# Optimization experiments

Measured on AMD Instinct MI355X. Metric: run time of the kernel, lower is better.

Reference implementation:

```python
import jax, jax.numpy as jnp
import numpy as np

LR = 0.1  # inner-loop learning rate from `param - 0.1 * grad`

D = 4096          # memory width d; key/val are (1, d) per docstring
CTX = 512         # loss_context_size: number of keys per update step


def setup_inputs() -> dict:
    key = jax.random.key(0)
    k1, k2, k3 = jax.random.split(key, 3)
    W = jax.random.normal(k1, (D, D), dtype=jnp.float32) / np.sqrt(D)
    keys = jax.random.normal(k2, (CTX, D), dtype=jnp.float32)
    vals = jax.random.normal(k3, (CTX, D), dtype=jnp.float32)
    return {"W": W, "keys": keys, "vals": vals}


def reference(W, keys, vals):
    # OneStep.forward: preds_i = functional_forward(key_i, (W,)) = key_i @ W,
    # loss = MSE(preds, vals); new_W = W - 0.1 * dloss/dW.
    # The per-key loop is batched into a single (CTX, D) x (D, D) matmul.
    def loss_fn(Wp):
        preds = keys @ Wp  # (CTX, D)
        return jnp.mean((preds - vals) ** 2)

    g = jax.grad(loss_fn)(W)
    return W - LR * g
```

## Files before the change

kernel.cpp:

```cpp
#include <hip/hip_runtime.h>
#include <hip/hip_bf16.h>


typedef __bf16 bf16_t;
typedef __bf16 bf16x8 __attribute__((ext_vector_type(8)));
typedef float f32x4 __attribute__((ext_vector_type(4)));

#define D_DIM 4096
#define CTX_N 512
#define UPD_SCALE 9.5367431640625e-8f

__device__ __forceinline__ void gld16(const bf16_t* g, bf16_t* l) {
    __builtin_amdgcn_global_load_lds(
        (const __attribute__((address_space(1))) void*)g,
        (__attribute__((address_space(3))) void*)l, 16, 0, 0);
}

__device__ __forceinline__ void t_body2(
    float* tile, const float* __restrict__ src, bf16_t* __restrict__ dstT,
    bf16_t* __restrict__ dstN, int M, int N, int bx, int by)
{
    const int tid = threadIdx.x;
    const int C0 = bx * 64, R0 = by * 64;
    const int r  = tid >> 2, cs = (tid & 3) * 16;

    const float* s = src + (size_t)(R0 + r) * N + C0 + cs;
    float f[16];
#pragma unroll
    for (int u = 0; u < 4; ++u) {
        const float4 v = ((const float4*)s)[u];
        f[4 * u + 0] = v.x; f[4 * u + 1] = v.y; f[4 * u + 2] = v.z; f[4 * u + 3] = v.w;
    }
#pragma unroll
    for (int u = 0; u < 16; ++u) tile[r * 65 + cs + u] = f[u];

    if (dstN) {
        bf16x8 v0, v1;
#pragma unroll
        for (int u = 0; u < 8; ++u) { v0[u] = (bf16_t)f[u]; v1[u] = (bf16_t)f[8 + u]; }
        bf16_t* d = dstN + (size_t)(R0 + r) * N + C0 + cs;
        *(bf16x8*)d = v0; *(bf16x8*)(d + 8) = v1;
    }
    __syncthreads();

    bf16x8 o0, o1;
#pragma unroll
    for (int u = 0; u < 8; ++u) {
        o0[u] = (bf16_t)tile[(cs + u) * 65 + r];
        o1[u] = (bf16_t)tile[(cs + 8 + u) * 65 + r];
    }
    bf16_t* d = dstT + (size_t)(C0 + r) * M + R0 + cs;
    *(bf16x8*)d = o0; *(bf16x8*)(d + 8) = o1;
}

__global__ __launch_bounds__(256) void t_all(
    const float* __restrict__ W, const float* __restrict__ K,
    const float* __restrict__ V, bf16_t* __restrict__ Wt,
    bf16_t* __restrict__ Kt, bf16_t* __restrict__ Kb, bf16_t* __restrict__ Vt)
{
    __shared__ float tile[64 * 65];
    const int y = blockIdx.y;
    if (y < 64)      t_body2(tile, W, Wt, nullptr, D_DIM, D_DIM, blockIdx.x, y);
    else if (y < 72) t_body2(tile, K, Kt, Kb,      CTX_N, D_DIM, blockIdx.x, y - 64);
    else             t_body2(tile, V, Vt, nullptr, CTX_N, D_DIM, blockIdx.x, y - 72);
}



__global__ __launch_bounds__(256, 2) void k1_residual(
    const bf16_t* __restrict__ Wt, const bf16_t* __restrict__ Kb,
    const bf16_t* __restrict__ Vt, bf16_t* __restrict__ Rt)
{
    __shared__ __align__(16) bf16_t stg[16384];

    const int tid = threadIdx.x, wave = tid >> 6, lane = tid & 63;
    const int j0 = blockIdx.x * 64, c0 = blockIdx.y * 64;
    const int l15 = lane & 15, quad = lane >> 4;
    const int wm = wave >> 1, wn = wave & 1;

    f32x4 acc[2][2] = {};

    const int rl = lane >> 3;
    const int sl = ((lane & 7) ^ rl) * 8;
    const bf16_t* gA0 = Wt + (size_t)(j0 + wave * 8      + rl) * D_DIM + sl;
    const bf16_t* gA1 = Wt + (size_t)(j0 + wave * 8 + 32 + rl) * D_DIM + sl;
    const bf16_t* gB0 = Kb + (size_t)(c0 + wave * 8      + rl) * D_DIM + sl;
    const bf16_t* gB1 = Kb + (size_t)(c0 + wave * 8 + 32 + rl) * D_DIM + sl;

    auto stage = [&](int bsel, int t) {
        bf16_t* buf = stg + bsel * 8192;
        gld16(gA0 + t * 64, buf + (size_t)wave * 512 + lane * 8);
        gld16(gA1 + t * 64, buf + (size_t)(wave + 4) * 512 + lane * 8);
        gld16(gB0 + t * 64, buf + 4096 + (size_t)wave * 512 + lane * 8);
        gld16(gB1 + t * 64, buf + 4096 + (size_t)(wave + 4) * 512 + lane * 8);
    };

#define K1_COMPUTE(BSEL)                                                     \
    {                                                                        \
        const bf16_t* buf = stg + (BSEL) * 8192;                             \
        const int r3 = l15 & 7, uh = l15 >> 3;                               \
        bf16x8 a[2][2], b[2][2];                                             \
        _Pragma("unroll")                                                    \
        for (int kk = 0; kk < 2; ++kk) {                                     \
            const int slot = r3 * 8 + ((kk * 4 + quad) ^ r3);                \
            _Pragma("unroll")                                                \
            for (int x = 0; x < 2; ++x) {                                    \
                const int uA = wm * 4 + x * 2 + uh;                          \
                const int uB = wn * 4 + x * 2 + uh;                          \
                a[x][kk] = *(const bf16x8*)(buf + uA * 512 + slot * 8);      \
                b[x][kk] = *(const bf16x8*)(buf + 4096 + uB * 512 + slot * 8); \
            }                                                                \
        }                                                                    \
        _Pragma("unroll")                                                    \
        for (int kk = 0; kk < 2; ++kk)                                       \
            _Pragma("unroll")                                                \
            for (int mi = 0; mi < 2; ++mi)                                   \
                _Pragma("unroll")                                            \
                for (int ni = 0; ni < 2; ++ni)                               \
                    acc[mi][ni] = __builtin_amdgcn_mfma_f32_16x16x32_bf16(   \
                        a[mi][kk], b[ni][kk], acc[mi][ni], 0, 0, 0);         \
    }

    stage(0, 0);
    __syncthreads();
#pragma unroll 1
    for (int t = 0; t < 62; t += 2) {
        stage(1, t + 1);
        __builtin_amdgcn_sched_barrier(0);
        K1_COMPUTE(0);
        __syncthreads();
        stage(0, t + 2);
        __builtin_amdgcn_sched_barrier(0);
        K1_COMPUTE(1);
        __syncthreads();
    }
    stage(1, 63);
    __builtin_amdgcn_sched_barrier(0);
    K1_COMPUTE(0);
    __syncthreads();
    K1_COMPUTE(1);

    {
        const size_t base =
            (size_t)(j0 + wm * 32 + quad * 4) * CTX_N + c0 + wn * 32 + l15;
#pragma unroll
        for (int mi = 0; mi < 2; ++mi)
#pragma unroll
            for (int r = 0; r < 4; ++r) {
                const size_t rowb = base + (size_t)(mi * 16 + r) * CTX_N;
#pragma unroll
                for (int ni = 0; ni < 2; ++ni) {
                    const size_t idx = rowb + ni * 16;
                    Rt[idx] = (bf16_t)(acc[mi][ni][r] - (float)Vt[idx]);
                }
            }
    }
}


#define K2_COMPUTE(BSEL)                                                     \
    {                                                                        \
        const bf16_t* As = (const bf16_t*)(smem + (BSEL) * 16384);           \
        const bf16_t* Bs = (const bf16_t*)(smem + (BSEL) * 16384 + 8192);    \
        bf16x8 af[4], bq[4];                                                 \
        _Pragma("unroll")                                                    \
        for (int mi = 0; mi < 4; ++mi)                                       \
            af[mi] = *(const bf16x8*)(As + (wi + mi * 16 + l15) * 32 + quad * 8); \
        _Pragma("unroll")                                                    \
        for (int ni = 0; ni < 4; ++ni)                                       \
            bq[ni] = *(const bf16x8*)(Bs + (wj + ni * 16 + l15) * 32 + quad * 8); \
        _Pragma("unroll")                                                    \
        for (int mi = 0; mi < 4; ++mi)                                       \
            _Pragma("unroll")                                                \
            for (int ni = 0; ni < 4; ++ni)                                   \
                acc[mi][ni] = __builtin_amdgcn_mfma_f32_16x16x32_bf16(       \
                    af[mi], bq[ni], acc[mi][ni], 0, 0, 0);                   \
    }

__global__ __launch_bounds__(256) void k2_update(
    const bf16_t* __restrict__ Kt, const bf16_t* __restrict__ Rt,
    const float* __restrict__ W, float* __restrict__ out)
{
    __shared__ __align__(16) char smem[32768];

    const int tid = threadIdx.x;

    const int id = blockIdx.x + 32 * blockIdx.y;
    const int xp = (id >> 3) & 31;
    const int yp = (id & 7) + 8 * (id >> 8);
    const int j0 = xp * 128, i0 = yp * 128;

    const int lane = tid & 63, wave = tid >> 6;
    const int wi = (wave >> 1) * 64, wj = (wave & 1) * 64;
    const int l15 = lane & 15, quad = lane >> 4;

    f32x4 acc[4][4] = {};

    const bf16_t* ga = Kt + (size_t)(i0 + (tid >> 2)) * CTX_N + (tid & 3) * 8;
    const bf16_t* gb = Rt + (size_t)(j0 + (tid >> 2)) * CTX_N + (tid & 3) * 8;

    auto stage = [&](int bsel, int cc) {
        bf16_t* la = (bf16_t*)(smem + bsel * 16384) + tid * 8;
        bf16_t* lb = (bf16_t*)(smem + bsel * 16384 + 8192) + tid * 8;
        gld16(ga + cc, la);
        gld16(ga + cc + (size_t)64 * CTX_N, la + 64 * 32);
        gld16(gb + cc, lb);
        gld16(gb + cc + (size_t)64 * CTX_N, lb + 64 * 32);
    };

    stage(0, 0);
    __syncthreads();
#pragma unroll 1
    for (int t = 1; t <= 13; t += 2) {
        stage(1, t * 32);
        __builtin_amdgcn_sched_barrier(0);
        K2_COMPUTE(0);
        __syncthreads();
        stage(0, (t + 1) * 32);
        __builtin_amdgcn_sched_barrier(0);
        K2_COMPUTE(1);
        __syncthreads();
    }
    stage(1, 15 * 32);
    __builtin_amdgcn_sched_barrier(0);
    K2_COMPUTE(0);
    __syncthreads();
    K2_COMPUTE(1);

    const size_t base = (size_t)(i0 + wi + quad * 4) * D_DIM + j0 + wj + l15;
    const float* wp = W + base;
    float*       op = out + base;

    float w0[16], w1[16];
#pragma unroll
    for (int r = 0; r < 4; ++r)
#pragma unroll
        for (int ni = 0; ni < 4; ++ni)
            w0[r * 4 + ni] = wp[(size_t)r * D_DIM + ni * 16];

#pragma unroll
    for (int mi = 0; mi < 4; ++mi) {
        float* wcur = (mi & 1) ? w1 : w0;
        float* wnxt = (mi & 1) ? w0 : w1;
        if (mi < 3) {
#pragma unroll
            for (int r = 0; r < 4; ++r)
#pragma unroll
                for (int ni = 0; ni < 4; ++ni)
                    wnxt[r * 4 + ni] =
                        wp[(size_t)((mi + 1) * 16 + r) * D_DIM + ni * 16];
        }
#pragma unroll
        for (int r = 0; r < 4; ++r)
#pragma unroll
            for (int ni = 0; ni < 4; ++ni)
                op[(size_t)(mi * 16 + r) * D_DIM + ni * 16] =
                    wcur[r * 4 + ni] - UPD_SCALE * acc[mi][ni][r];
    }
}

extern "C" void kernel_launch(void* const* d_in, const int* in_sizes, int n_in,
                              void* d_out, int out_size, void* d_ws, size_t ws_size,
                              hipStream_t stream) {
    const float* W = (const float*)d_in[0];
    const float* K = (const float*)d_in[1];
    const float* V = (const float*)d_in[2];
    float* out = (float*)d_out;

    char* ws = (char*)d_ws;
    bf16_t* Wt = (bf16_t*)(ws);
    bf16_t* Kt = (bf16_t*)(ws + (size_t)32 * 1024 * 1024);
    bf16_t* Kb = (bf16_t*)(ws + (size_t)36 * 1024 * 1024);
    bf16_t* Vt = (bf16_t*)(ws + (size_t)40 * 1024 * 1024);
    bf16_t* Rt = (bf16_t*)(ws + (size_t)44 * 1024 * 1024);

    t_all      <<<dim3(64, 80), 256, 0, stream>>>(W, K, V, Wt, Kt, Kb, Vt);
    k1_residual<<<dim3(64, 8),  256, 0, stream>>>(Wt, Kb, Vt, Rt);
    k2_update  <<<dim3(32, 32), 256, 0, stream>>>(Kt, Rt, W, out);
}
```

Baseline: 193.8 us.

## Enlarge k2 update tile to 256x128 with 512 threads and XOR-swizzled LDS

The rank-update GEMM kernel now has each block cover 256 rows of the key dimension instead of 128, using 8 waves (512 threads) and half as many blocks. Staging now uses per-wave 16-row chunks with an XOR swizzle on the 16-byte column slot, so the LDS fragment reads avoid bank conflicts. Each B (residual) tile staged into LDS is shared by more rows, and LDS per block drops relative to the tile size. The launch-bounds change to (512,2) limits registers and may cause spills. Because the epilogue and the indexing code are not shown, the block-to-tile mapping with the new 16-row grid may be inconsistent.

Result: no change. 193.0 us (-0.4%).

```diff
diff --git a/kernel.cpp b/kernel.cpp
--- a/kernel.cpp
+++ b/kernel.cpp
@@ -158,37 +158,40 @@
 }
 
 
-#define K2_COMPUTE(BSEL)                                                     \
-    {                                                                        \
-        const bf16_t* As = (const bf16_t*)(smem + (BSEL) * 16384);           \
-        const bf16_t* Bs = (const bf16_t*)(smem + (BSEL) * 16384 + 8192);    \
-        bf16x8 af[4], bq[4];                                                 \
-        _Pragma("unroll")                                                    \
-        for (int mi = 0; mi < 4; ++mi)                                       \
-            af[mi] = *(const bf16x8*)(As + (wi + mi * 16 + l15) * 32 + quad * 8); \
-        _Pragma("unroll")                                                    \
-        for (int ni = 0; ni < 4; ++ni)                                       \
-            bq[ni] = *(const bf16x8*)(Bs + (wj + ni * 16 + l15) * 32 + quad * 8); \
-        _Pragma("unroll")                                                    \
-        for (int mi = 0; mi < 4; ++mi)                                       \
-            _Pragma("unroll")                                                \
-            for (int ni = 0; ni < 4; ++ni)                                   \
-                acc[mi][ni] = __builtin_amdgcn_mfma_f32_16x16x32_bf16(       \
-                    af[mi], bq[ni], acc[mi][ni], 0, 0, 0);                   \
-    }
-
-__global__ __launch_bounds__(256) void k2_update(
+#define K2_COMPUTE(BSEL)                                                      \
+    {                                                                         \
+        const bf16_t* bufA = stg + (BSEL) * 12288;                            \
+        const bf16_t* bufB = bufA + 8192;                                     \
+        const int sgx = (quad ^ (l15 & 3)) * 8;                               \
+        bf16x8 af[4], bq[4];                                                  \
+        _Pragma("unroll")                                                     \
+        for (int mi = 0; mi < 4; ++mi)                                        \
+            af[mi] = *(const bf16x8*)(                                        \
+                bufA + ((wave >> 1) * 4 + mi) * 512 + l15 * 32 + sgx);        \
+        _Pragma("unroll")                                                     \
+        for (int ni = 0; ni < 4; ++ni)                                        \
+            bq[ni] = *(const bf16x8*)(                                        \
+                bufB + ((wave & 1) * 4 + ni) * 512 + l15 * 32 + sgx);         \
+        _Pragma("unroll")                                                     \
+        for (int mi = 0; mi < 4; ++mi)                                        \
+            _Pragma("unroll")                                                 \
+            for (int ni = 0; ni < 4; ++ni)                                    \
+                acc[mi][ni] = __builtin_amdgcn_mfma_f32_16x16x32_bf16(        \
+                    af[mi], bq[ni], acc[mi][ni], 0, 0, 0);                    \
+    }
+
+__global__ __launch_bounds__(512, 2) void k2_update(
     const bf16_t* __restrict__ Kt, const bf16_t* __restrict__ Rt,
     const float* __restrict__ W, float* __restrict__ out)
 {
-    __shared__ __align__(16) char smem[32768];
+    __shared__ __align__(16) bf16_t stg[2 * 12288];
 
     const int tid = threadIdx.x;
 
     const int id = blockIdx.x + 32 * blockIdx.y;
     const int xp = (id >> 3) & 31;
     const int yp = (id & 7) + 8 * (id >> 8);
-    const int j0 = xp * 128, i0 = yp * 128;
+    const int j0 = xp * 128, i0 = yp * 256;
 
     const int lane = tid & 63, wave = tid >> 6;
     const int wi = (wave >> 1) * 64, wj = (wave & 1) * 64;
@@ -196,16 +199,17 @@
 
     f32x4 acc[4][4] = {};
 
-    const bf16_t* ga = Kt + (size_t)(i0 + (tid >> 2)) * CTX_N + (tid & 3) * 8;
-    const bf16_t* gb = Rt + (size_t)(j0 + (tid >> 2)) * CTX_N + (tid & 3) * 8;
+    const int rl = lane >> 2;
+    const int sl = ((lane & 3) ^ (rl & 3)) * 8;
+    const bf16_t* gA0 = Kt + (size_t)(i0 + wave * 16       + rl) * CTX_N + sl;
+    const bf16_t* gA1 = Kt + (size_t)(i0 + wave * 16 + 128 + rl) * CTX_N + sl;
+    const bf16_t* gB0 = Rt + (size_t)(j0 + wave * 16       + rl) * CTX_N + sl;
 
     auto stage = [&](int bsel, int cc) {
-        bf16_t* la = (bf16_t*)(smem + bsel * 16384) + tid * 8;
-        bf16_t* lb = (bf16_t*)(smem + bsel * 16384 + 8192) + tid * 8;
-        gld16(ga + cc, la);
-        gld16(ga + cc + (size_t)64 * CTX_N, la + 64 * 32);
-        gld16(gb + cc, lb);
-        gld16(gb + cc + (size_t)64 * CTX_N, lb + 64 * 32);
+        bf16_t* buf = stg + bsel * 12288;
+        gld16(gA0 + cc, buf + (size_t)wave * 512 + lane * 8);
+        gld16(gA1 + cc, buf + (size_t)(wave + 8) * 512 + lane * 8);
+        gld16(gB0 + cc, buf + 8192 + (size_t)wave * 512 + lane * 8);
     };
 
     stage(0, 0);
@@ -276,5 +280,5 @@
 
     t_all      <<<dim3(64, 80), 256, 0, stream>>>(W, K, V, Wt, Kt, Kb, Vt);
     k1_residual<<<dim3(64, 8),  256, 0, stream>>>(Wt, Kb, Vt, Rt);
-    k2_update  <<<dim3(32, 32), 256, 0, stream>>>(Kt, Rt, W, out);
-}
+    k2_update  <<<dim3(32, 16), 512, 0, stream>>>(Kt, Rt, W, out);
+}
```
